# Kernel tuning notes

Hardware: AMD Instinct MI355X
Metric: run time of the kernel (lower is better)

Reference implementation:

```python
import jax, jax.numpy as jnp
import numpy as np

B, S, D_IN, D_EMB = 8, 2048, 512, 512

def setup_inputs() -> dict:
    key = jax.random.key(0)
    ks = jax.random.split(key, 7)
    s = 1.0 / np.sqrt(D_IN)
    return {
        "x": jax.random.normal(ks[0], (B, S, D_IN), dtype=jnp.float32),
        "Wq": jax.random.uniform(ks[1], (D_IN, D_EMB), jnp.float32, -s, s),
        "bq": jax.random.uniform(ks[2], (D_EMB,), jnp.float32, -s, s),
        "Wk": jax.random.uniform(ks[3], (D_IN, D_EMB), jnp.float32, -s, s),
        "bk": jax.random.uniform(ks[4], (D_EMB,), jnp.float32, -s, s),
        "Wv": jax.random.uniform(ks[5], (D_IN, D_EMB), jnp.float32, -s, s),
        "bv": jax.random.uniform(ks[6], (D_EMB,), jnp.float32, -s, s),
    }

def reference(x, Wq, bq, Wk, bk, Wv, bv):
    # single-head attention: softmax(QK^T / sqrt(d)) V
    q = x @ Wq + bq            # [B,S,E]
    k = x @ Wk + bk
    v = x @ Wv + bv
    scores = jnp.einsum('bse,bte->bst', q, k) / jnp.sqrt(jnp.float32(D_EMB))
    attn = jax.nn.softmax(scores, axis=-1)  # [B,S,S]
    return jnp.einsum('bst,bte->bse', attn, v)
```

## Files before the change

### kernel.cpp

```cpp
#include <hip/hip_runtime.h>
#include <stdint.h>


using f32x4 = __attribute__((ext_vector_type(4))) float;
using s16x8 = __attribute__((ext_vector_type(8))) short;
using u16x4 = __attribute__((ext_vector_type(4))) unsigned short;

#define S_LEN 2048
#define EMB   512

#define ASYNC16(g, l)                                                     \
  __builtin_amdgcn_global_load_lds(                                       \
      (const __attribute__((address_space(1))) void*)(g),                 \
      (__attribute__((address_space(3))) void*)(l), 16, 0, 0)

__device__ __forceinline__ unsigned short f2bf(float f) {
  union { float f; unsigned u; } v; v.f = f;
  unsigned r = v.u + 0x7fffu + ((v.u >> 16) & 1u);
  return (unsigned short)(r >> 16);
}

__global__ __launch_bounds__(256) void xconv_kernel(
    const float* __restrict__ x, short* __restrict__ xb) {
  int i = (blockIdx.x * 256 + threadIdx.x) * 8;
  f32x4 a = *(const f32x4*)(x + i);
  f32x4 b = *(const f32x4*)(x + i + 4);
  s16x8 h;
  h[0] = (short)f2bf(a[0]); h[1] = (short)f2bf(a[1]);
  h[2] = (short)f2bf(a[2]); h[3] = (short)f2bf(a[3]);
  h[4] = (short)f2bf(b[0]); h[5] = (short)f2bf(b[1]);
  h[6] = (short)f2bf(b[2]); h[7] = (short)f2bf(b[3]);
  *(s16x8*)(xb + i) = h;
}

__global__ __launch_bounds__(256) void wconv_kernel(
    const float* __restrict__ Wq, const float* __restrict__ Wk,
    const float* __restrict__ Wv, short* __restrict__ Wt) {
  int idx = blockIdx.x * 256 + threadIdx.x;
  int mat = idx >> 18;
  int r   = idx & 262143;
  int n   = r >> 9;
  int k   = r & 511;
  const float* W = (mat == 0) ? Wq : (mat == 1) ? Wk : Wv;
  Wt[idx] = (short)f2bf(W[k * 512 + n]);
}

__global__ __launch_bounds__(256) void qkv_gemm(
    const short* __restrict__ xb, const short* __restrict__ Wt,
    const float* __restrict__ bq, const float* __restrict__ bk,
    const float* __restrict__ bv,
    short* __restrict__ Qg, short* __restrict__ Kg, short* __restrict__ VTg) {
  __shared__ __align__(16) short As[128 * 64];
  __shared__ __align__(16) short Bs[128 * 64];
  int gid = blockIdx.x;
  int mat = gid >> 9;
  int rem = gid & 511;
  int mt  = rem & 127, nt = rem >> 7;
  int m0  = mt << 7,   n0 = nt << 7;
  const short* W    = Wt + (size_t)mat * 262144;
  const float* bias = (mat == 0) ? bq : (mat == 1) ? bk : bv;

  int tid = threadIdx.x, lane = tid & 63, wv = tid >> 6;
  int l16 = lane & 15, quad = lane >> 4;
  int wr = (wv & 1) << 6, wc = (wv >> 1) << 6;
  int drow = lane >> 3;
  int dchk = (lane & 7) ^ drow;

  const f32x4 Z4 = {0.f, 0.f, 0.f, 0.f};
  f32x4 acc[4][4];
#pragma unroll
  for (int a = 0; a < 4; ++a)
#pragma unroll
    for (int c = 0; c < 4; ++c) acc[a][c] = Z4;

  for (int it = 0; it < 8; ++it) {
    int k0 = it << 6;
    __syncthreads();
#pragma unroll
    for (int i = 0; i < 4; ++i) {
      int g   = wv * 4 + i;
      int row = g * 8 + drow;
      ASYNC16(xb + (size_t)(m0 + row) * 512 + k0 + dchk * 8, &As[g * 512]);
    }
#pragma unroll
    for (int i = 0; i < 4; ++i) {
      int g   = wv * 4 + i;
      int row = g * 8 + drow;
      ASYNC16(W + (size_t)(n0 + row) * 512 + k0 + dchk * 8, &Bs[g * 512]);
    }
    __syncthreads();
#pragma unroll
    for (int kk = 0; kk < 2; ++kk) {
      s16x8 af[4], bfr[4];
#pragma unroll
      for (int rb = 0; rb < 4; ++rb) {
        int row = wr + rb * 16 + l16;
        int c   = kk * 4 + quad;
        af[rb] = *(const s16x8*)(As + row * 64 + ((c ^ (row & 7)) * 8));
      }
#pragma unroll
      for (int cb = 0; cb < 4; ++cb) {
        int row = wc + cb * 16 + l16;
        int c   = kk * 4 + quad;
        bfr[cb] = *(const s16x8*)(Bs + row * 64 + ((c ^ (row & 7)) * 8));
      }
#pragma unroll
      for (int rb = 0; rb < 4; ++rb)
#pragma unroll
        for (int cb = 0; cb < 4; ++cb)
          acc[rb][cb] = __builtin_amdgcn_mfma_f32_16x16x32_bf16(af[rb], bfr[cb], acc[rb][cb], 0, 0, 0);
    }
  }

  float bsv[4];
#pragma unroll
  for (int cb = 0; cb < 4; ++cb) bsv[cb] = bias[n0 + wc + cb * 16 + l16];

  if (mat < 2) {
    short* D = (mat == 0) ? Qg : Kg;
#pragma unroll
    for (int rb = 0; rb < 4; ++rb)
#pragma unroll
      for (int cb = 0; cb < 4; ++cb)
#pragma unroll
        for (int r = 0; r < 4; ++r) {
          int m = m0 + wr + rb * 16 + quad * 4 + r;
          D[(size_t)m * 512 + n0 + wc + cb * 16 + l16] =
              (short)f2bf(acc[rb][cb][r] + bsv[cb]);
        }
  } else {
#pragma unroll
    for (int rb = 0; rb < 4; ++rb)
#pragma unroll
      for (int cb = 0; cb < 4; ++cb) {
        u16x4 h;
#pragma unroll
        for (int r = 0; r < 4; ++r) h[r] = f2bf(acc[rb][cb][r] + bsv[cb]);
        int m  = m0 + wr + rb * 16 + quad * 4;
        int bb = m >> 11, s = m & 2047;
        int e  = n0 + wc + cb * 16 + l16;
        size_t idx = ((((size_t)bb * 32 + (e >> 4)) * 64 + (s >> 5)) * 16 +
                      (e & 15)) * 32 + (s & 31);
        *(u16x4*)(VTg + idx) = h;
      }
  }
}

__global__ __launch_bounds__(512, 2) void attn_kernel(
    const short* __restrict__ Qg, const short* __restrict__ Kg,
    const short* __restrict__ VTg, float* __restrict__ out) {
  __shared__ __align__(16) short Kt[32 * 512];
  __shared__ __align__(16) short Pl[64 * 40];
  __shared__ float l_l[64];
  const float SCL2 = 0.06375871855f;

  int b = blockIdx.x & 7, qt = blockIdx.x >> 3;
  int s0 = qt << 6;
  int tid = threadIdx.x, lane = tid & 63, wv = tid >> 6;
  int l16 = lane & 15, quad = lane >> 4;
  int a = wv & 3, h = wv >> 2;
  int e0 = wv << 6;

  const short* Kb = Kg  + (size_t)b * S_LEN * 512;
  const short* Vb = VTg + (size_t)b * 1048576;

  const short* kdma[4];
#pragma unroll
  for (int i = 0; i < 4; ++i) {
    int r = wv * 4 + i;
    kdma[i] = Kb + (size_t)r * 512 + ((lane ^ (r & 7)) * 8);
  }
  const short* vbase = Vb + (size_t)wv * 131072 + l16 * 32 + quad * 8;

#pragma unroll
  for (int i = 0; i < 4; ++i)
    ASYNC16(kdma[i], &Kt[(wv * 4 + i) * 512]);

  const short* qrow = Qg + ((size_t)b * S_LEN + s0 + a * 16 + l16) * 512 + quad * 8;
  s16x8 qf[16];
#pragma unroll
  for (int kk = 0; kk < 16; ++kk) qf[kk] = *(const s16x8*)(qrow + kk * 32);

  const f32x4 Z4 = {0.f, 0.f, 0.f, 0.f};
  f32x4 acc[4][4];
#pragma unroll
  for (int rb = 0; rb < 4; ++rb)
#pragma unroll
    for (int cb = 0; cb < 4; ++cb) acc[rb][cb] = Z4;
  f32x4 lsum = Z4;

  __syncthreads();

  for (int kt = 0; kt < 64; ++kt) {
    s16x8 vf[4];
#pragma unroll
    for (int cb = 0; cb < 4; ++cb)
      vf[cb] = *(const s16x8*)(vbase + cb * 32768 + kt * 512);

    f32x4 s_a = Z4, s_b = Z4;
    int krow = h * 16 + l16;
    const short* kb = &Kt[krow * 512];
    int ksw = krow & 7;
#pragma unroll
    for (int kk = 0; kk < 8; ++kk) {
      s16x8 kf0 = *(const s16x8*)(kb + (((2 * kk) * 4 + quad) ^ ksw) * 8);
      s_a = __builtin_amdgcn_mfma_f32_16x16x32_bf16(qf[2 * kk], kf0, s_a, 0, 0, 0);
      s16x8 kf1 = *(const s16x8*)(kb + (((2 * kk + 1) * 4 + quad) ^ ksw) * 8);
      s_b = __builtin_amdgcn_mfma_f32_16x16x32_bf16(qf[2 * kk + 1], kf1, s_b, 0, 0, 0);
    }
    f32x4 sv = s_a + s_b;

#pragma unroll
    for (int r = 0; r < 4; ++r) {
      float p = exp2f(sv[r] * SCL2);
      lsum[r] += p;
      Pl[(a * 16 + quad * 4 + r) * 40 + h * 16 + l16] = (short)f2bf(p);
    }

    __syncthreads();

    if (kt + 1 < 64) {
      size_t adv = (size_t)(kt + 1) * 16384;
#pragma unroll
      for (int i = 0; i < 4; ++i)
        ASYNC16(kdma[i] + adv, &Kt[(wv * 4 + i) * 512]);
    }

    s16x8 pf[4];
#pragma unroll
    for (int rb = 0; rb < 4; ++rb)
      pf[rb] = *(const s16x8*)(&Pl[(rb * 16 + l16) * 40 + quad * 8]);
#pragma unroll
    for (int cb = 0; cb < 4; ++cb)
#pragma unroll
      for (int rb = 0; rb < 4; ++rb)
        acc[rb][cb] = __builtin_amdgcn_mfma_f32_16x16x32_bf16(pf[rb], vf[cb], acc[rb][cb], 0, 0, 0);

    __syncthreads();
  }

#pragma unroll
  for (int r = 0; r < 4; ++r) {
    float v = lsum[r];
    v += __shfl_xor(v, 1);
    v += __shfl_xor(v, 2);
    v += __shfl_xor(v, 4);
    v += __shfl_xor(v, 8);
    lsum[r] = v;
  }
  if (h == 0 && l16 == 0) {
#pragma unroll
    for (int r = 0; r < 4; ++r) l_l[a * 16 + quad * 4 + r] = lsum[r];
  }
  __syncthreads();
  if (h == 1 && l16 == 0) {
#pragma unroll
    for (int r = 0; r < 4; ++r) l_l[a * 16 + quad * 4 + r] += lsum[r];
  }
  __syncthreads();

#pragma unroll
  for (int rb = 0; rb < 4; ++rb) {
    f32x4 lv = *(const f32x4*)(l_l + rb * 16 + quad * 4);
    f32x4 li;
#pragma unroll
    for (int r = 0; r < 4; ++r) li[r] = 1.0f / lv[r];
#pragma unroll
    for (int cb = 0; cb < 4; ++cb)
#pragma unroll
      for (int r = 0; r < 4; ++r)
        out[((size_t)b * S_LEN + s0 + rb * 16 + quad * 4 + r) * 512 + e0 + cb * 16 + l16] =
            acc[rb][cb][r] * li[r];
  }
}

extern "C" void kernel_launch(void* const* d_in, const int* in_sizes, int n_in,
                              void* d_out, int out_size, void* d_ws, size_t ws_size,
                              hipStream_t stream) {
  const float* x  = (const float*)d_in[0];
  const float* Wq = (const float*)d_in[1];
  const float* bq = (const float*)d_in[2];
  const float* Wk = (const float*)d_in[3];
  const float* bk = (const float*)d_in[4];
  const float* Wv = (const float*)d_in[5];
  const float* bv = (const float*)d_in[6];

  short* Wt  = (short*)d_ws;
  short* xb  = (short*)((char*)d_ws + 1572864);
  short* Qg  = xb + (size_t)8388608;
  short* Kg  = Qg + (size_t)8388608;
  short* VTg = Kg + (size_t)8388608;

  xconv_kernel<<<4096, 256, 0, stream>>>(x, xb);
  wconv_kernel<<<3072, 256, 0, stream>>>(Wq, Wk, Wv, Wt);
  qkv_gemm<<<1536, 256, 0, stream>>>(xb, Wt, bq, bk, bv, Qg, Kg, VTg);
  attn_kernel<<<256, 512, 0, stream>>>(Qg, Kg, VTg, (float*)d_out);
}
```

Before: 241.1 us.

## Restructure attention to 32x32 MFMA with Q in LDS and fragment-tiled K/V layouts

The attention kernel now keeps the 64-row Q tile in swizzled LDS and streams K and V directly from global memory in fragment-ready tiled layouts, which the QKV GEMM writes out. Each wave handles a 256-key chunk using 32x32x16 MFMAs, with double-buffered P in LDS, instead of per-32-key iterations with K staged through LDS. The weight transpose kernel now uses an LDS tile to get coalesced reads and writes. The aim is fewer barriers and LDS round trips per key block and denser MFMA use, at the cost of uncoalesced scalar K stores in the GEMM epilogue and more register pressure.

New measurement: 296.1 us. 22.8% more time.

```diff
diff --git a/kernel.cpp b/kernel.cpp
--- a/kernel.cpp
+++ b/kernel.cpp
@@ -2,9 +2,10 @@
 #include <stdint.h>
 
 
-using f32x4 = __attribute__((ext_vector_type(4))) float;
-using s16x8 = __attribute__((ext_vector_type(8))) short;
-using u16x4 = __attribute__((ext_vector_type(4))) unsigned short;
+using f32x4  = __attribute__((ext_vector_type(4))) float;
+using f32x16 = __attribute__((ext_vector_type(16))) float;
+using s16x8  = __attribute__((ext_vector_type(8))) short;
+using u16x4  = __attribute__((ext_vector_type(4))) unsigned short;
 
 #define S_LEN 2048
 #define EMB   512
@@ -36,13 +37,31 @@
 __global__ __launch_bounds__(256) void wconv_kernel(
     const float* __restrict__ Wq, const float* __restrict__ Wk,
     const float* __restrict__ Wv, short* __restrict__ Wt) {
-  int idx = blockIdx.x * 256 + threadIdx.x;
-  int mat = idx >> 18;
-  int r   = idx & 262143;
-  int n   = r >> 9;
-  int k   = r & 511;
+  __shared__ float T[64][65];
+  int bid = blockIdx.x;
+  int mat = bid >> 6;
+  int t   = bid & 63;
+  int k0  = (t & 7) << 6, n0 = (t >> 3) << 6;
   const float* W = (mat == 0) ? Wq : (mat == 1) ? Wk : Wv;
-  Wt[idx] = (short)f2bf(W[k * 512 + n]);
+  int tid = threadIdx.x;
+  int rr = tid >> 4, cc = tid & 15;
+#pragma unroll
+  for (int p = 0; p < 4; ++p) {
+    int row = p * 16 + rr;
+    f32x4 v = *(const f32x4*)(W + (size_t)(k0 + row) * 512 + n0 + cc * 4);
+#pragma unroll
+    for (int j = 0; j < 4; ++j) T[row][cc * 4 + j] = v[j];
+  }
+  __syncthreads();
+  short* D = Wt + (size_t)mat * 262144;
+#pragma unroll
+  for (int p = 0; p < 4; ++p) {
+    int nrow = p * 16 + rr;
+    u16x4 h;
+#pragma unroll
+    for (int j = 0; j < 4; ++j) h[j] = f2bf(T[cc * 4 + j][nrow]);
+    *(u16x4*)(D + (size_t)(n0 + nrow) * 512 + k0 + cc * 4) = h;
+  }
 }
 
 __global__ __launch_bounds__(256) void qkv_gemm(
@@ -116,8 +135,7 @@
 #pragma unroll
   for (int cb = 0; cb < 4; ++cb) bsv[cb] = bias[n0 + wc + cb * 16 + l16];
 
-  if (mat < 2) {
-    short* D = (mat == 0) ? Qg : Kg;
+  if (mat == 0) {
 #pragma unroll
     for (int rb = 0; rb < 4; ++rb)
 #pragma unroll
@@ -125,9 +143,23 @@
 #pragma unroll
         for (int r = 0; r < 4; ++r) {
           int m = m0 + wr + rb * 16 + quad * 4 + r;
-          D[(size_t)m * 512 + n0 + wc + cb * 16 + l16] =
+          Qg[(size_t)m * 512 + n0 + wc + cb * 16 + l16] =
               (short)f2bf(acc[rb][cb][r] + bsv[cb]);
         }
+  } else if (mat == 1) {
+#pragma unroll
+    for (int rb = 0; rb < 4; ++rb)
+#pragma unroll
+      for (int cb = 0; cb < 4; ++cb)
+#pragma unroll
+        for (int r = 0; r < 4; ++r) {
+          int m  = m0 + wr + rb * 16 + quad * 4 + r;
+          int bb = m >> 11, sl = m & 2047;
+          int e  = n0 + wc + cb * 16 + l16;
+          size_t idx = (((size_t)bb * 64 + (sl >> 5)) * 32 + (e >> 4)) * 512 +
+                       (sl & 31) * 16 + (e & 15);
+          Kg[idx] = (short)f2bf(acc[rb][cb][r] + bsv[cb]);
+        }
   } else {
 #pragma unroll
     for (int rb = 0; rb < 4; ++rb)
@@ -137,10 +169,10 @@
 #pragma unroll
         for (int r = 0; r < 4; ++r) h[r] = f2bf(acc[rb][cb][r] + bsv[cb]);
         int m  = m0 + wr + rb * 16 + quad * 4;
-        int bb = m >> 11, s = m & 2047;
+        int bb = m >> 11, sl = m & 2047;
         int e  = n0 + wc + cb * 16 + l16;
-        size_t idx = ((((size_t)bb * 32 + (e >> 4)) * 64 + (s >> 5)) * 16 +
-                      (e & 15)) * 32 + (s & 31);
+        size_t idx = (((size_t)bb * 16 + (e >> 5)) * 128 + (sl >> 4)) * 512 +
+                     (e & 31) * 16 + (sl & 15);
         *(u16x4*)(VTg + idx) = h;
       }
   }
@@ -149,129 +181,142 @@
 __global__ __launch_bounds__(512, 2) void attn_kernel(
     const short* __restrict__ Qg, const short* __restrict__ Kg,
     const short* __restrict__ VTg, float* __restrict__ out) {
-  __shared__ __align__(16) short Kt[32 * 512];
-  __shared__ __align__(16) short Pl[64 * 40];
-  __shared__ float l_l[64];
+  __shared__ __align__(16) short Qs[64 * 512];
+  __shared__ __align__(16) short Pl[2][64 * 256];
+  __shared__ float lred[8 * 64];
   const float SCL2 = 0.06375871855f;
 
   int b = blockIdx.x & 7, qt = blockIdx.x >> 3;
   int s0 = qt << 6;
   int tid = threadIdx.x, lane = tid & 63, wv = tid >> 6;
-  int l16 = lane & 15, quad = lane >> 4;
-  int a = wv & 3, h = wv >> 2;
-  int e0 = wv << 6;
-
-  const short* Kb = Kg  + (size_t)b * S_LEN * 512;
+  int l5 = lane & 31, hh = lane >> 5;
+
+  const short* Qb = Qg  + ((size_t)b * S_LEN + s0) * 512;
+  const short* Kb = Kg  + (size_t)b * 1048576;
   const short* Vb = VTg + (size_t)b * 1048576;
 
-  const short* kdma[4];
-#pragma unroll
-  for (int i = 0; i < 4; ++i) {
-    int r = wv * 4 + i;
-    kdma[i] = Kb + (size_t)r * 512 + ((lane ^ (r & 7)) * 8);
-  }
-  const short* vbase = Vb + (size_t)wv * 131072 + l16 * 32 + quad * 8;
-
-#pragma unroll
-  for (int i = 0; i < 4; ++i)
-    ASYNC16(kdma[i], &Kt[(wv * 4 + i) * 512]);
-
-  const short* qrow = Qg + ((size_t)b * S_LEN + s0 + a * 16 + l16) * 512 + quad * 8;
-  s16x8 qf[16];
-#pragma unroll
-  for (int kk = 0; kk < 16; ++kk) qf[kk] = *(const s16x8*)(qrow + kk * 32);
-
-  const f32x4 Z4 = {0.f, 0.f, 0.f, 0.f};
-  f32x4 acc[4][4];
-#pragma unroll
-  for (int rb = 0; rb < 4; ++rb)
-#pragma unroll
-    for (int cb = 0; cb < 4; ++cb) acc[rb][cb] = Z4;
-  f32x4 lsum = Z4;
+#pragma unroll
+  for (int i = 0; i < 8; ++i) {
+    int row = wv * 8 + i;
+    s16x8 v = *(const s16x8*)(Qb + (size_t)row * 512 + lane * 8);
+    *(s16x8*)(Qs + row * 512 + ((lane ^ (row & 7)) * 8)) = v;
+  }
+
+  const f32x16 Z16 = {0.f,0.f,0.f,0.f,0.f,0.f,0.f,0.f,0.f,0.f,0.f,0.f,0.f,0.f,0.f,0.f};
+  f32x16 Oa[2][2];
+  Oa[0][0] = Z16; Oa[0][1] = Z16; Oa[1][0] = Z16; Oa[1][1] = Z16;
+  float lsum[2][16];
+#pragma unroll
+  for (int rg = 0; rg < 2; ++rg)
+#pragma unroll
+    for (int r = 0; r < 16; ++r) lsum[rg][r] = 0.f;
+
+  int fragoff = l5 * 16 + hh * 8;
+  int swz0 = l5 & 7;
 
   __syncthreads();
 
-  for (int kt = 0; kt < 64; ++kt) {
-    s16x8 vf[4];
-#pragma unroll
-    for (int cb = 0; cb < 4; ++cb)
-      vf[cb] = *(const s16x8*)(vbase + cb * 32768 + kt * 512);
-
-    f32x4 s_a = Z4, s_b = Z4;
-    int krow = h * 16 + l16;
-    const short* kb = &Kt[krow * 512];
-    int ksw = krow & 7;
-#pragma unroll
-    for (int kk = 0; kk < 8; ++kk) {
-      s16x8 kf0 = *(const s16x8*)(kb + (((2 * kk) * 4 + quad) ^ ksw) * 8);
-      s_a = __builtin_amdgcn_mfma_f32_16x16x32_bf16(qf[2 * kk], kf0, s_a, 0, 0, 0);
-      s16x8 kf1 = *(const s16x8*)(kb + (((2 * kk + 1) * 4 + quad) ^ ksw) * 8);
-      s_b = __builtin_amdgcn_mfma_f32_16x16x32_bf16(qf[2 * kk + 1], kf1, s_b, 0, 0, 0);
-    }
-    f32x4 sv = s_a + s_b;
-
-#pragma unroll
-    for (int r = 0; r < 4; ++r) {
-      float p = exp2f(sv[r] * SCL2);
-      lsum[r] += p;
-      Pl[(a * 16 + quad * 4 + r) * 40 + h * 16 + l16] = (short)f2bf(p);
+  for (int it = 0; it < 8; ++it) {
+    int cur = it & 1;
+
+    f32x16 S0 = Z16, S1 = Z16;
+    const short* kbase = Kb + (size_t)((it * 8 + wv) * 32) * 512 + fragoff;
+    s16x8 kf[8];
+#pragma unroll
+    for (int ks = 0; ks < 8; ++ks) kf[ks] = *(const s16x8*)(kbase + ks * 512);
+#pragma unroll
+    for (int ks = 0; ks < 32; ++ks) {
+      int ch = ((ks * 2 + hh) ^ swz0) * 8;
+      s16x8 qa0 = *(const s16x8*)(Qs + l5 * 512 + ch);
+      s16x8 qa1 = *(const s16x8*)(Qs + (32 + l5) * 512 + ch);
+      S0 = __builtin_amdgcn_mfma_f32_32x32x16_bf16(qa0, kf[ks & 7], S0, 0, 0, 0);
+      S1 = __builtin_amdgcn_mfma_f32_32x32x16_bf16(qa1, kf[ks & 7], S1, 0, 0, 0);
+      if (ks < 24) kf[ks & 7] = *(const s16x8*)(kbase + (ks + 8) * 512);
+    }
+
+    short* Pc = &Pl[cur][0];
+#pragma unroll
+    for (int r = 0; r < 16; ++r) {
+      int rbase = (r & 3) + 8 * (r >> 2) + 4 * hh;
+      int chunk = wv * 4 + (l5 >> 3);
+      {
+        float p = exp2f(S0[r] * SCL2);
+        lsum[0][r] += p;
+        int prow = rbase;
+        Pc[prow * 256 + ((chunk ^ (prow & 7)) * 8) + (l5 & 7)] = (short)f2bf(p);
+      }
+      {
+        float p = exp2f(S1[r] * SCL2);
+        lsum[1][r] += p;
+        int prow = 32 + rbase;
+        Pc[prow * 256 + ((chunk ^ (prow & 7)) * 8) + (l5 & 7)] = (short)f2bf(p);
+      }
     }
 
     __syncthreads();
 
-    if (kt + 1 < 64) {
-      size_t adv = (size_t)(kt + 1) * 16384;
-#pragma unroll
-      for (int i = 0; i < 4; ++i)
-        ASYNC16(kdma[i] + adv, &Kt[(wv * 4 + i) * 512]);
-    }
-
-    s16x8 pf[4];
-#pragma unroll
-    for (int rb = 0; rb < 4; ++rb)
-      pf[rb] = *(const s16x8*)(&Pl[(rb * 16 + l16) * 40 + quad * 8]);
-#pragma unroll
-    for (int cb = 0; cb < 4; ++cb)
-#pragma unroll
-      for (int rb = 0; rb < 4; ++rb)
-        acc[rb][cb] = __builtin_amdgcn_mfma_f32_16x16x32_bf16(pf[rb], vf[cb], acc[rb][cb], 0, 0, 0);
-
-    __syncthreads();
-  }
-
-#pragma unroll
-  for (int r = 0; r < 4; ++r) {
-    float v = lsum[r];
-    v += __shfl_xor(v, 1);
-    v += __shfl_xor(v, 2);
-    v += __shfl_xor(v, 4);
-    v += __shfl_xor(v, 8);
-    lsum[r] = v;
-  }
-  if (h == 0 && l16 == 0) {
-#pragma unroll
-    for (int r = 0; r < 4; ++r) l_l[a * 16 + quad * 4 + r] = lsum[r];
+    const short* vb0 = Vb + (size_t)((wv * 2 + 0) * 128 + it * 16) * 512 + fragoff;
+    const short* vb1 = Vb + (size_t)((wv * 2 + 1) * 128 + it * 16) * 512 + fragoff;
+    s16x8 vf[8];
+#pragma unroll
+    for (int k4 = 0; k4 < 4; ++k4) {
+      vf[k4 * 2]     = *(const s16x8*)(vb0 + k4 * 512);
+      vf[k4 * 2 + 1] = *(const s16x8*)(vb1 + k4 * 512);
+    }
+#pragma unroll
+    for (int ks = 0; ks < 16; ++ks) {
+      int ch = ((ks * 2 + hh) ^ swz0) * 8;
+      s16x8 pa0 = *(const s16x8*)(Pc + l5 * 256 + ch);
+      s16x8 pa1 = *(const s16x8*)(Pc + (32 + l5) * 256 + ch);
+      Oa[0][0] = __builtin_amdgcn_mfma_f32_32x32x16_bf16(pa0, vf[(ks & 3) * 2], Oa[0][0], 0, 0, 0);
+      Oa[1][0] = __builtin_amdgcn_mfma_f32_32x32x16_bf16(pa1, vf[(ks & 3) * 2], Oa[1][0], 0, 0, 0);
+      Oa[0][1] = __builtin_amdgcn_mfma_f32_32x32x16_bf16(pa0, vf[(ks & 3) * 2 + 1], Oa[0][1], 0, 0, 0);
+      Oa[1][1] = __builtin_amdgcn_mfma_f32_32x32x16_bf16(pa1, vf[(ks & 3) * 2 + 1], Oa[1][1], 0, 0, 0);
+      if (ks < 12) {
+        vf[(ks & 3) * 2]     = *(const s16x8*)(vb0 + (ks + 4) * 512);
+        vf[(ks & 3) * 2 + 1] = *(const s16x8*)(vb1 + (ks + 4) * 512);
+      }
+    }
+  }
+
+#pragma unroll
+  for (int rg = 0; rg < 2; ++rg)
+#pragma unroll
+    for (int r = 0; r < 16; ++r) {
+      float v = lsum[rg][r];
+      v += __shfl_xor(v, 1);
+      v += __shfl_xor(v, 2);
+      v += __shfl_xor(v, 4);
+      v += __shfl_xor(v, 8);
+      v += __shfl_xor(v, 16);
+      lsum[rg][r] = v;
+    }
+  if (l5 == 0) {
+#pragma unroll
+    for (int rg = 0; rg < 2; ++rg)
+#pragma unroll
+      for (int r = 0; r < 16; ++r)
+        lred[wv * 64 + rg * 32 + (r & 3) + 8 * (r >> 2) + 4 * hh] = lsum[rg][r];
   }
   __syncthreads();
-  if (h == 1 && l16 == 0) {
-#pragma unroll
-    for (int r = 0; r < 4; ++r) l_l[a * 16 + quad * 4 + r] += lsum[r];
+  if (tid < 64) {
+    float t = 0.f;
+#pragma unroll
+    for (int w = 0; w < 8; ++w) t += lred[w * 64 + tid];
+    lred[tid] = 1.0f / t;
   }
   __syncthreads();
 
-#pragma unroll
-  for (int rb = 0; rb < 4; ++rb) {
-    f32x4 lv = *(const f32x4*)(l_l + rb * 16 + quad * 4);
-    f32x4 li;
-#pragma unroll
-    for (int r = 0; r < 4; ++r) li[r] = 1.0f / lv[r];
-#pragma unroll
-    for (int cb = 0; cb < 4; ++cb)
-#pragma unroll
-      for (int r = 0; r < 4; ++r)
-        out[((size_t)b * S_LEN + s0 + rb * 16 + quad * 4 + r) * 512 + e0 + cb * 16 + l16] =
-            acc[rb][cb][r] * li[r];
-  }
+  float* ob = out + ((size_t)b * S_LEN + s0) * 512;
+#pragma unroll
+  for (int rg = 0; rg < 2; ++rg)
+#pragma unroll
+    for (int r = 0; r < 16; ++r) {
+      int row = rg * 32 + (r & 3) + 8 * (r >> 2) + 4 * hh;
+      float li = lred[row];
+      ob[(size_t)row * 512 + wv * 64 + l5]      = Oa[rg][0][r] * li;
+      ob[(size_t)row * 512 + wv * 64 + 32 + l5] = Oa[rg][1][r] * li;
+    }
 }
 
 extern "C" void kernel_launch(void* const* d_in, const int* in_sizes, int n_in,
@@ -292,7 +337,7 @@
   short* VTg = Kg + (size_t)8388608;
 
   xconv_kernel<<<4096, 256, 0, stream>>>(x, xb);
-  wconv_kernel<<<3072, 256, 0, stream>>>(Wq, Wk, Wv, Wt);
+  wconv_kernel<<<192, 256, 0, stream>>>(Wq, Wk, Wv, Wt);
   qkv_gemm<<<1536, 256, 0, stream>>>(xb, Wt, bq, bk, bv, Qg, Kg, VTg);
   attn_kernel<<<256, 512, 0, stream>>>(Qg, Kg, VTg, (float*)d_out);
 }
```

## Double K tile per attention step and tile weight transpose through LDS

Applied to the files above, without the earlier changes.

The attention kernel now loads 64 key rows per iteration instead of 32, halving the loop trip count and the number of barriers. The wave mapping is remapped so each wave computes scores for two 16-row query groups against one 16-key slice, reusing each K fragment across two MFMAs. A four-way LDS reduction combines the row sums. The weight conversion kernel now transposes through a padded shared-memory tile, giving coalesced reads and vector writes. The cost is doubled LDS for K, a wider P buffer and more registers for the two query fragment sets, which may hurt occupancy under the 512x2 launch bound.

New measurement: 264.7 us. 9.8% more time.

```diff
diff --git a/kernel.cpp b/kernel.cpp
--- a/kernel.cpp
+++ b/kernel.cpp
@@ -36,13 +36,31 @@
 __global__ __launch_bounds__(256) void wconv_kernel(
     const float* __restrict__ Wq, const float* __restrict__ Wk,
     const float* __restrict__ Wv, short* __restrict__ Wt) {
-  int idx = blockIdx.x * 256 + threadIdx.x;
-  int mat = idx >> 18;
-  int r   = idx & 262143;
-  int n   = r >> 9;
-  int k   = r & 511;
+  __shared__ float T[64][65];
+  int bid = blockIdx.x;
+  int mat = bid >> 6;
+  int t   = bid & 63;
+  int k0  = (t & 7) << 6, n0 = (t >> 3) << 6;
   const float* W = (mat == 0) ? Wq : (mat == 1) ? Wk : Wv;
-  Wt[idx] = (short)f2bf(W[k * 512 + n]);
+  int tid = threadIdx.x;
+  int rr = tid >> 4, cc = tid & 15;
+#pragma unroll
+  for (int p = 0; p < 4; ++p) {
+    int row = p * 16 + rr;
+    f32x4 v = *(const f32x4*)(W + (size_t)(k0 + row) * 512 + n0 + cc * 4);
+#pragma unroll
+    for (int j = 0; j < 4; ++j) T[row][cc * 4 + j] = v[j];
+  }
+  __syncthreads();
+  short* D = Wt + (size_t)mat * 262144;
+#pragma unroll
+  for (int p = 0; p < 4; ++p) {
+    int nrow = p * 16 + rr;
+    u16x4 h;
+#pragma unroll
+    for (int j = 0; j < 4; ++j) h[j] = f2bf(T[cc * 4 + j][nrow]);
+    *(u16x4*)(D + (size_t)(n0 + nrow) * 512 + k0 + cc * 4) = h;
+  }
 }
 
 __global__ __launch_bounds__(256) void qkv_gemm(
@@ -137,10 +155,10 @@
 #pragma unroll
         for (int r = 0; r < 4; ++r) h[r] = f2bf(acc[rb][cb][r] + bsv[cb]);
         int m  = m0 + wr + rb * 16 + quad * 4;
-        int bb = m >> 11, s = m & 2047;
+        int bb = m >> 11, sl = m & 2047;
         int e  = n0 + wc + cb * 16 + l16;
-        size_t idx = ((((size_t)bb * 32 + (e >> 4)) * 64 + (s >> 5)) * 16 +
-                      (e & 15)) * 32 + (s & 31);
+        size_t idx = ((((size_t)bb * 32 + (e >> 4)) * 64 + (sl >> 5)) * 16 +
+                      (e & 15)) * 32 + (sl & 31);
         *(u16x4*)(VTg + idx) = h;
       }
   }
@@ -149,129 +167,150 @@
 __global__ __launch_bounds__(512, 2) void attn_kernel(
     const short* __restrict__ Qg, const short* __restrict__ Kg,
     const short* __restrict__ VTg, float* __restrict__ out) {
-  __shared__ __align__(16) short Kt[32 * 512];
-  __shared__ __align__(16) short Pl[64 * 40];
-  __shared__ float l_l[64];
+  __shared__ __align__(16) short Kt[64 * 512];
+  __shared__ __align__(16) short Pl[64 * 72];
+  __shared__ float lred[4][64];
   const float SCL2 = 0.06375871855f;
 
   int b = blockIdx.x & 7, qt = blockIdx.x >> 3;
   int s0 = qt << 6;
   int tid = threadIdx.x, lane = tid & 63, wv = tid >> 6;
   int l16 = lane & 15, quad = lane >> 4;
-  int a = wv & 3, h = wv >> 2;
+  int a = wv >> 2, h = wv & 3;
   int e0 = wv << 6;
 
   const short* Kb = Kg  + (size_t)b * S_LEN * 512;
   const short* Vb = VTg + (size_t)b * 1048576;
 
-  const short* kdma[4];
-#pragma unroll
-  for (int i = 0; i < 4; ++i) {
-    int r = wv * 4 + i;
-    kdma[i] = Kb + (size_t)r * 512 + ((lane ^ (r & 7)) * 8);
-  }
-  const short* vbase = Vb + (size_t)wv * 131072 + l16 * 32 + quad * 8;
-
-#pragma unroll
-  for (int i = 0; i < 4; ++i)
-    ASYNC16(kdma[i], &Kt[(wv * 4 + i) * 512]);
-
-  const short* qrow = Qg + ((size_t)b * S_LEN + s0 + a * 16 + l16) * 512 + quad * 8;
-  s16x8 qf[16];
-#pragma unroll
-  for (int kk = 0; kk < 16; ++kk) qf[kk] = *(const s16x8*)(qrow + kk * 32);
+  const short* kg0 = Kb + (size_t)(wv * 8) * 512;
+  int klo = lane;
+
+  const short* vbase = Vb + (size_t)(wv * 4) * 32768 + l16 * 32 + quad * 8;
+
+#pragma unroll
+  for (int i = 0; i < 8; ++i)
+    ASYNC16(kg0 + (size_t)i * 512 + ((klo ^ i) * 8), &Kt[(wv * 8 + i) * 512]);
+
+  const short* qrowA = Qg + ((size_t)b * S_LEN + s0 + a * 32 + l16) * 512 + quad * 8;
+  const short* qrowB = qrowA + (size_t)16 * 512;
+  s16x8 qfA[16], qfB[16];
+#pragma unroll
+  for (int c = 0; c < 16; ++c) {
+    qfA[c] = *(const s16x8*)(qrowA + c * 32);
+    qfB[c] = *(const s16x8*)(qrowB + c * 32);
+  }
 
   const f32x4 Z4 = {0.f, 0.f, 0.f, 0.f};
   f32x4 acc[4][4];
 #pragma unroll
-  for (int rb = 0; rb < 4; ++rb)
-#pragma unroll
-    for (int cb = 0; cb < 4; ++cb) acc[rb][cb] = Z4;
-  f32x4 lsum = Z4;
+  for (int g = 0; g < 4; ++g)
+#pragma unroll
+    for (int ec = 0; ec < 4; ++ec) acc[g][ec] = Z4;
+  f32x4 lsumA = Z4, lsumB = Z4;
 
   __syncthreads();
 
-  for (int kt = 0; kt < 64; ++kt) {
-    s16x8 vf[4];
-#pragma unroll
-    for (int cb = 0; cb < 4; ++cb)
-      vf[cb] = *(const s16x8*)(vbase + cb * 32768 + kt * 512);
-
-    f32x4 s_a = Z4, s_b = Z4;
+  for (int it = 0; it < 32; ++it) {
+    const short* vb_it = vbase + (size_t)(it * 2) * 512;
+    s16x8 vf0[4];
+#pragma unroll
+    for (int ec = 0; ec < 4; ++ec)
+      vf0[ec] = *(const s16x8*)(vb_it + (size_t)ec * 32768);
+
+    f32x4 sA = Z4, sB = Z4;
     int krow = h * 16 + l16;
     const short* kb = &Kt[krow * 512];
     int ksw = krow & 7;
 #pragma unroll
-    for (int kk = 0; kk < 8; ++kk) {
-      s16x8 kf0 = *(const s16x8*)(kb + (((2 * kk) * 4 + quad) ^ ksw) * 8);
-      s_a = __builtin_amdgcn_mfma_f32_16x16x32_bf16(qf[2 * kk], kf0, s_a, 0, 0, 0);
-      s16x8 kf1 = *(const s16x8*)(kb + (((2 * kk + 1) * 4 + quad) ^ ksw) * 8);
-      s_b = __builtin_amdgcn_mfma_f32_16x16x32_bf16(qf[2 * kk + 1], kf1, s_b, 0, 0, 0);
-    }
-    f32x4 sv = s_a + s_b;
+    for (int c = 0; c < 16; ++c) {
+      s16x8 kf = *(const s16x8*)(kb + (((c * 4 + quad) ^ ksw) * 8));
+      sA = __builtin_amdgcn_mfma_f32_16x16x32_bf16(qfA[c], kf, sA, 0, 0, 0);
+      sB = __builtin_amdgcn_mfma_f32_16x16x32_bf16(qfB[c], kf, sB, 0, 0, 0);
+    }
 
 #pragma unroll
     for (int r = 0; r < 4; ++r) {
-      float p = exp2f(sv[r] * SCL2);
-      lsum[r] += p;
-      Pl[(a * 16 + quad * 4 + r) * 40 + h * 16 + l16] = (short)f2bf(p);
+      float pA = exp2f(sA[r] * SCL2);
+      lsumA[r] += pA;
+      Pl[(a * 32 + quad * 4 + r) * 72 + h * 16 + l16] = (short)f2bf(pA);
+      float pB = exp2f(sB[r] * SCL2);
+      lsumB[r] += pB;
+      Pl[(a * 32 + 16 + quad * 4 + r) * 72 + h * 16 + l16] = (short)f2bf(pB);
     }
 
     __syncthreads();
 
-    if (kt + 1 < 64) {
-      size_t adv = (size_t)(kt + 1) * 16384;
-#pragma unroll
-      for (int i = 0; i < 4; ++i)
-        ASYNC16(kdma[i] + adv, &Kt[(wv * 4 + i) * 512]);
+    if (it + 1 < 32) {
+      size_t adv = (size_t)(it + 1) * 32768;
+#pragma unroll
+      for (int i = 0; i < 8; ++i)
+        ASYNC16(kg0 + adv + (size_t)i * 512 + ((klo ^ i) * 8),
+                &Kt[(wv * 8 + i) * 512]);
     }
 
     s16x8 pf[4];
 #pragma unroll
-    for (int rb = 0; rb < 4; ++rb)
-      pf[rb] = *(const s16x8*)(&Pl[(rb * 16 + l16) * 40 + quad * 8]);
-#pragma unroll
-    for (int cb = 0; cb < 4; ++cb)
-#pragma unroll
-      for (int rb = 0; rb < 4; ++rb)
-        acc[rb][cb] = __builtin_amdgcn_mfma_f32_16x16x32_bf16(pf[rb], vf[cb], acc[rb][cb], 0, 0, 0);
+    for (int g = 0; g < 4; ++g)
+      pf[g] = *(const s16x8*)(&Pl[(g * 16 + l16) * 72 + quad * 8]);
+#pragma unroll
+    for (int ec = 0; ec < 4; ++ec)
+#pragma unroll
+      for (int g = 0; g < 4; ++g)
+        acc[g][ec] = __builtin_amdgcn_mfma_f32_16x16x32_bf16(pf[g], vf0[ec], acc[g][ec], 0, 0, 0);
+
+    s16x8 vf1[4];
+    const short* vb1 = vb_it + 512;
+#pragma unroll
+    for (int ec = 0; ec < 4; ++ec)
+      vf1[ec] = *(const s16x8*)(vb1 + (size_t)ec * 32768);
+#pragma unroll
+    for (int g = 0; g < 4; ++g)
+      pf[g] = *(const s16x8*)(&Pl[(g * 16 + l16) * 72 + 32 + quad * 8]);
+#pragma unroll
+    for (int ec = 0; ec < 4; ++ec)
+#pragma unroll
+      for (int g = 0; g < 4; ++g)
+        acc[g][ec] = __builtin_amdgcn_mfma_f32_16x16x32_bf16(pf[g], vf1[ec], acc[g][ec], 0, 0, 0);
 
     __syncthreads();
   }
 
 #pragma unroll
   for (int r = 0; r < 4; ++r) {
-    float v = lsum[r];
-    v += __shfl_xor(v, 1);
-    v += __shfl_xor(v, 2);
-    v += __shfl_xor(v, 4);
-    v += __shfl_xor(v, 8);
-    lsum[r] = v;
-  }
-  if (h == 0 && l16 == 0) {
-#pragma unroll
-    for (int r = 0; r < 4; ++r) l_l[a * 16 + quad * 4 + r] = lsum[r];
+    float vA = lsumA[r];
+    vA += __shfl_xor(vA, 1); vA += __shfl_xor(vA, 2);
+    vA += __shfl_xor(vA, 4); vA += __shfl_xor(vA, 8);
+    lsumA[r] = vA;
+    float vB = lsumB[r];
+    vB += __shfl_xor(vB, 1); vB += __shfl_xor(vB, 2);
+    vB += __shfl_xor(vB, 4); vB += __shfl_xor(vB, 8);
+    lsumB[r] = vB;
+  }
+  if (l16 == 0) {
+#pragma unroll
+    for (int r = 0; r < 4; ++r) {
+      lred[h][a * 32 + quad * 4 + r]      = lsumA[r];
+      lred[h][a * 32 + 16 + quad * 4 + r] = lsumB[r];
+    }
   }
   __syncthreads();
-  if (h == 1 && l16 == 0) {
-#pragma unroll
-    for (int r = 0; r < 4; ++r) l_l[a * 16 + quad * 4 + r] += lsum[r];
+  if (tid < 64) {
+    float t = lred[0][tid] + lred[1][tid] + lred[2][tid] + lred[3][tid];
+    lred[0][tid] = 1.0f / t;
   }
   __syncthreads();
 
-#pragma unroll
-  for (int rb = 0; rb < 4; ++rb) {
-    f32x4 lv = *(const f32x4*)(l_l + rb * 16 + quad * 4);
-    f32x4 li;
-#pragma unroll
-    for (int r = 0; r < 4; ++r) li[r] = 1.0f / lv[r];
-#pragma unroll
-    for (int cb = 0; cb < 4; ++cb)
-#pragma unroll
-      for (int r = 0; r < 4; ++r)
-        out[((size_t)b * S_LEN + s0 + rb * 16 + quad * 4 + r) * 512 + e0 + cb * 16 + l16] =
-            acc[rb][cb][r] * li[r];
-  }
+  float* ob = out + ((size_t)b * S_LEN + s0) * 512 + e0;
+#pragma unroll
+  for (int g = 0; g < 4; ++g)
+#pragma unroll
+    for (int r = 0; r < 4; ++r) {
+      float li = lred[0][g * 16 + quad * 4 + r];
+#pragma unroll
+      for (int ec = 0; ec < 4; ++ec)
+        ob[(size_t)(g * 16 + quad * 4 + r) * 512 + ec * 16 + l16] =
+            acc[g][ec][r] * li;
+    }
 }
 
 extern "C" void kernel_launch(void* const* d_in, const int* in_sizes, int n_in,
@@ -292,7 +331,7 @@
   short* VTg = Kg + (size_t)8388608;
 
   xconv_kernel<<<4096, 256, 0, stream>>>(x, xb);
-  wconv_kernel<<<3072, 256, 0, stream>>>(Wq, Wk, Wv, Wt);
+  wconv_kernel<<<192, 256, 0, stream>>>(Wq, Wk, Wv, Wt);
   qkv_gemm<<<1536, 256, 0, stream>>>(xb, Wt, bq, bk, bv, Qg, Kg, VTg);
   attn_kernel<<<256, 512, 0, stream>>>(Qg, Kg, VTg, (float*)d_out);
 }
```

## Triple-buffer K tiles, double-buffer P, and tile the weight transpose

Applied to the files above, without the earlier changes.

The attention kernel now keeps three K tile buffers in LDS, prefetching two tiles ahead, and double-buffers the P tile. This lets the loop use one barrier per iteration with a manual vmcnt wait instead of two __syncthreads, and setprio is raised around the MFMA blocks. The weight conversion kernel is rewritten to transpose through a shared-memory tile with coalesced vector loads and stores instead of strided scalar reads. The cost is more LDS per block, which may limit occupancy at two blocks per CU, and a hand-written waitcnt count that has to match the number of outstanding loads.

New measurement: 240.2 us. No clear change (-0.4%).

```diff
diff --git a/kernel.cpp b/kernel.cpp
--- a/kernel.cpp
+++ b/kernel.cpp
@@ -36,13 +36,31 @@
 __global__ __launch_bounds__(256) void wconv_kernel(
     const float* __restrict__ Wq, const float* __restrict__ Wk,
     const float* __restrict__ Wv, short* __restrict__ Wt) {
-  int idx = blockIdx.x * 256 + threadIdx.x;
-  int mat = idx >> 18;
-  int r   = idx & 262143;
-  int n   = r >> 9;
-  int k   = r & 511;
+  __shared__ float T[64][65];
+  int bid = blockIdx.x;
+  int mat = bid >> 6;
+  int t   = bid & 63;
+  int k0  = (t & 7) << 6, n0 = (t >> 3) << 6;
   const float* W = (mat == 0) ? Wq : (mat == 1) ? Wk : Wv;
-  Wt[idx] = (short)f2bf(W[k * 512 + n]);
+  int tid = threadIdx.x;
+  int rr = tid >> 4, cc = tid & 15;
+#pragma unroll
+  for (int p = 0; p < 4; ++p) {
+    int row = p * 16 + rr;
+    f32x4 v = *(const f32x4*)(W + (size_t)(k0 + row) * 512 + n0 + cc * 4);
+#pragma unroll
+    for (int j = 0; j < 4; ++j) T[row][cc * 4 + j] = v[j];
+  }
+  __syncthreads();
+  short* D = Wt + (size_t)mat * 262144;
+#pragma unroll
+  for (int p = 0; p < 4; ++p) {
+    int nrow = p * 16 + rr;
+    u16x4 h;
+#pragma unroll
+    for (int j = 0; j < 4; ++j) h[j] = f2bf(T[cc * 4 + j][nrow]);
+    *(u16x4*)(D + (size_t)(n0 + nrow) * 512 + k0 + cc * 4) = h;
+  }
 }
 
 __global__ __launch_bounds__(256) void qkv_gemm(
@@ -137,10 +155,10 @@
 #pragma unroll
         for (int r = 0; r < 4; ++r) h[r] = f2bf(acc[rb][cb][r] + bsv[cb]);
         int m  = m0 + wr + rb * 16 + quad * 4;
-        int bb = m >> 11, s = m & 2047;
+        int bb = m >> 11, sl = m & 2047;
         int e  = n0 + wc + cb * 16 + l16;
-        size_t idx = ((((size_t)bb * 32 + (e >> 4)) * 64 + (s >> 5)) * 16 +
-                      (e & 15)) * 32 + (s & 31);
+        size_t idx = ((((size_t)bb * 32 + (e >> 4)) * 64 + (sl >> 5)) * 16 +
+                      (e & 15)) * 32 + (sl & 31);
         *(u16x4*)(VTg + idx) = h;
       }
   }
@@ -149,8 +167,8 @@
 __global__ __launch_bounds__(512, 2) void attn_kernel(
     const short* __restrict__ Qg, const short* __restrict__ Kg,
     const short* __restrict__ VTg, float* __restrict__ out) {
-  __shared__ __align__(16) short Kt[32 * 512];
-  __shared__ __align__(16) short Pl[64 * 40];
+  __shared__ __align__(16) short Kt[3][32 * 512];
+  __shared__ __align__(16) short Pl[2][64 * 40];
   __shared__ float l_l[64];
   const float SCL2 = 0.06375871855f;
 
@@ -174,7 +192,10 @@
 
 #pragma unroll
   for (int i = 0; i < 4; ++i)
-    ASYNC16(kdma[i], &Kt[(wv * 4 + i) * 512]);
+    ASYNC16(kdma[i], &Kt[0][(wv * 4 + i) * 512]);
+#pragma unroll
+  for (int i = 0; i < 4; ++i)
+    ASYNC16(kdma[i] + 16384, &Kt[1][(wv * 4 + i) * 512]);
 
   const short* qrow = Qg + ((size_t)b * S_LEN + s0 + a * 16 + l16) * 512 + quad * 8;
   s16x8 qf[16];
@@ -191,16 +212,27 @@
 
   __syncthreads();
 
+  int rbuf = 0, wbuf = 2;
   for (int kt = 0; kt < 64; ++kt) {
     s16x8 vf[4];
 #pragma unroll
     for (int cb = 0; cb < 4; ++cb)
-      vf[cb] = *(const s16x8*)(vbase + cb * 32768 + kt * 512);
+      vf[cb] = *(const s16x8*)(vbase + (size_t)cb * 32768 + (size_t)kt * 512);
+    __builtin_amdgcn_sched_barrier(0);
+
+    {
+      size_t adv = (size_t)((kt + 2) & 63) * 16384;
+#pragma unroll
+      for (int i = 0; i < 4; ++i)
+        ASYNC16(kdma[i] + adv, &Kt[wbuf][(wv * 4 + i) * 512]);
+    }
+    __builtin_amdgcn_sched_barrier(0);
 
     f32x4 s_a = Z4, s_b = Z4;
     int krow = h * 16 + l16;
-    const short* kb = &Kt[krow * 512];
+    const short* kb = &Kt[rbuf][krow * 512];
     int ksw = krow & 7;
+    __builtin_amdgcn_s_setprio(1);
 #pragma unroll
     for (int kk = 0; kk < 8; ++kk) {
       s16x8 kf0 = *(const s16x8*)(kb + (((2 * kk) * 4 + quad) ^ ksw) * 8);
@@ -208,35 +240,33 @@
       s16x8 kf1 = *(const s16x8*)(kb + (((2 * kk + 1) * 4 + quad) ^ ksw) * 8);
       s_b = __builtin_amdgcn_mfma_f32_16x16x32_bf16(qf[2 * kk + 1], kf1, s_b, 0, 0, 0);
     }
+    __builtin_amdgcn_s_setprio(0);
     f32x4 sv = s_a + s_b;
 
+    short* Pc = Pl[kt & 1];
 #pragma unroll
     for (int r = 0; r < 4; ++r) {
       float p = exp2f(sv[r] * SCL2);
       lsum[r] += p;
-      Pl[(a * 16 + quad * 4 + r) * 40 + h * 16 + l16] = (short)f2bf(p);
-    }
-
-    __syncthreads();
-
-    if (kt + 1 < 64) {
-      size_t adv = (size_t)(kt + 1) * 16384;
-#pragma unroll
-      for (int i = 0; i < 4; ++i)
-        ASYNC16(kdma[i] + adv, &Kt[(wv * 4 + i) * 512]);
-    }
+      Pc[(a * 16 + quad * 4 + r) * 40 + h * 16 + l16] = (short)f2bf(p);
+    }
+
+    asm volatile("s_waitcnt vmcnt(8) lgkmcnt(0)\n\ts_barrier" ::: "memory");
 
     s16x8 pf[4];
 #pragma unroll
-    for (int rb = 0; rb < 4; ++rb)
-      pf[rb] = *(const s16x8*)(&Pl[(rb * 16 + l16) * 40 + quad * 8]);
+    for (int g = 0; g < 4; ++g)
+      pf[g] = *(const s16x8*)(Pc + (g * 16 + l16) * 40 + quad * 8);
+    __builtin_amdgcn_s_setprio(1);
 #pragma unroll
     for (int cb = 0; cb < 4; ++cb)
 #pragma unroll
-      for (int rb = 0; rb < 4; ++rb)
-        acc[rb][cb] = __builtin_amdgcn_mfma_f32_16x16x32_bf16(pf[rb], vf[cb], acc[rb][cb], 0, 0, 0);
-
-    __syncthreads();
+      for (int g = 0; g < 4; ++g)
+        acc[g][cb] = __builtin_amdgcn_mfma_f32_16x16x32_bf16(pf[g], vf[cb], acc[g][cb], 0, 0, 0);
+    __builtin_amdgcn_s_setprio(0);
+
+    rbuf = (rbuf == 2) ? 0 : rbuf + 1;
+    wbuf = (wbuf == 2) ? 0 : wbuf + 1;
   }
 
 #pragma unroll
@@ -292,7 +322,7 @@
   short* VTg = Kg + (size_t)8388608;
 
   xconv_kernel<<<4096, 256, 0, stream>>>(x, xb);
-  wconv_kernel<<<3072, 256, 0, stream>>>(Wq, Wk, Wv, Wt);
+  wconv_kernel<<<192, 256, 0, stream>>>(Wq, Wk, Wv, Wt);
   qkv_gemm<<<1536, 256, 0, stream>>>(xb, Wt, bq, bk, bv, Qg, Kg, VTg);
   attn_kernel<<<256, 512, 0, stream>>>(Qg, Kg, VTg, (float*)d_out);
 }
```
